# Kernel optimization log

Measured on AMD Instinct MI355X. Metric: run time of the kernel, lower is better.

The kernel has to match this reference:

```python
import jax, jax.numpy as jnp
import numpy as np

N_NODES = 50000
N_EDGES = 1600000
N_FEAT = 128
HIDDEN = 128
N_GRAPHS = 64
N_CLASSES = 10
N_REGS = 1


def setup_inputs() -> dict:
    key = jax.random.key(0)
    ks = jax.random.split(key, 16)
    inp = {
        "x": jax.random.normal(ks[0], (N_NODES, N_FEAT), dtype=jnp.float32),
        "edge_index": jax.random.randint(ks[1], (2, N_EDGES), 0, N_NODES, dtype=jnp.int32),
        "batch": jnp.sort(jax.random.randint(ks[2], (N_NODES,), 0, N_GRAPHS, dtype=jnp.int32)),
        # GCNConv layer params (PyG: linear without bias applied first, bias added after aggregation)
        "w0": jax.random.normal(ks[3], (N_FEAT, HIDDEN), dtype=jnp.float32) * 0.05,
        "b0": jax.random.normal(ks[4], (HIDDEN,), dtype=jnp.float32) * 0.05,
        "w1": jax.random.normal(ks[5], (HIDDEN, HIDDEN), dtype=jnp.float32) * 0.05,
        "b1": jax.random.normal(ks[6], (HIDDEN,), dtype=jnp.float32) * 0.05,
        "w2": jax.random.normal(ks[7], (HIDDEN, HIDDEN), dtype=jnp.float32) * 0.05,
        "b2": jax.random.normal(ks[8], (HIDDEN,), dtype=jnp.float32) * 0.05,
        # heads
        "wc": jax.random.normal(ks[9], (HIDDEN, N_CLASSES), dtype=jnp.float32) * 0.05,
        "bc": jax.random.normal(ks[10], (N_CLASSES,), dtype=jnp.float32) * 0.05,
        "wr": jax.random.normal(ks[11], (HIDDEN, N_REGS), dtype=jnp.float32) * 0.05,
        "br": jax.random.normal(ks[12], (N_REGS,), dtype=jnp.float32) * 0.05,
    }
    return inp


def _gcn_layer(x, src, dst, w, b, deg_inv_sqrt, deg_inv):
    # x: [N, Din] -> [N, Dout]. GCNConv: D^-1/2 (A+I) D^-1/2 (x W) + b
    h = x @ w  # [N, Dout]
    coef = (deg_inv_sqrt[src] * deg_inv_sqrt[dst])[:, None]  # [E, 1]
    agg = jax.ops.segment_sum(h[src] * coef, dst, num_segments=x.shape[0])
    agg = agg + h * deg_inv[:, None]  # self-loop term: deg^-1 * h
    return agg + b


def reference(x, edge_index, batch, w0, b0, w1, b1, w2, b2, wc, bc, wr, br):
    src, dst = edge_index[0], edge_index[1]
    n = x.shape[0]
    # degrees include self-loop weight 1 (PyG gcn_norm with edge_weight=1)
    deg = jax.ops.segment_sum(jnp.ones(src.shape, x.dtype), dst, num_segments=n) + 1.0
    deg_inv_sqrt = deg ** -0.5
    deg_inv = 1.0 / deg

    h = _gcn_layer(x, src, dst, w0, b0, deg_inv_sqrt, deg_inv)
    h = _gcn_layer(jax.nn.elu(h), src, dst, w1, b1, deg_inv_sqrt, deg_inv)
    h = _gcn_layer(jax.nn.elu(h), src, dst, w2, b2, deg_inv_sqrt, deg_inv)

    # global mean pool over graphs
    sums = jax.ops.segment_sum(h, batch, num_segments=N_GRAPHS)  # [G, H]
    cnt = jax.ops.segment_sum(jnp.ones((n,), h.dtype), batch, num_segments=N_GRAPHS)
    pooled = sums / jnp.maximum(cnt, 1.0)[:, None]

    cls_out = pooled @ wc + bc
    reg_out = pooled @ wr + br
    return (pooled, cls_out, reg_out)
```

## Files before the change

### kernel.cpp

```cpp
#include <hip/hip_runtime.h>
#include <hip/hip_fp16.h>
#include <math.h>

#define N_NODES   50000
#define N_EDGES   1600000
#define NF        128
#define N_GRAPHS  64
#define N_CLASSES 10

#define NBK       391
#define BK_SHIFT  7
#define BK_NODES  128
#define CHUNK     8192
#define NCHUNKS   ((N_EDGES + CHUNK - 1) / CHUNK)

typedef _Float16 half8 __attribute__((ext_vector_type(8)));
typedef float f32x4 __attribute__((ext_vector_type(4)));

__global__ void k_zero(int* __restrict__ bucket_cnt, float* __restrict__ sums) {
    int i = blockIdx.x * 256 + threadIdx.x;
    if (i < NBK) bucket_cnt[i] = 0;
    if (i < N_GRAPHS * NF) sums[i] = 0.f;
}

__global__ __launch_bounds__(256) void k_bcount(const int* __restrict__ dst,
                                                int* __restrict__ bucket_cnt) {
    __shared__ int h[NBK];
    int t = threadIdx.x;
    for (int i = t; i < NBK; i += 256) h[i] = 0;
    __syncthreads();
    int base = blockIdx.x * CHUNK;
    int end = min(base + CHUNK, N_EDGES);
    for (int e = base + t; e < end; e += 256)
        atomicAdd(&h[dst[e] >> BK_SHIFT], 1);
    __syncthreads();
    for (int i = t; i < NBK; i += 256)
        if (h[i]) atomicAdd(&bucket_cnt[i], h[i]);
}

__global__ __launch_bounds__(512) void k_bscan(const int* __restrict__ bucket_cnt,
                                               int* __restrict__ bucket_off,
                                               int* __restrict__ bucket_cursor,
                                               int* __restrict__ row_start) {
    __shared__ int ts[512];
    int t = threadIdx.x;
    int v = (t < NBK) ? bucket_cnt[t] : 0;
    ts[t] = v;
    __syncthreads();
    for (int off = 1; off < 512; off <<= 1) {
        int y = (t >= off) ? ts[t - off] : 0;
        __syncthreads();
        ts[t] += y;
        __syncthreads();
    }
    if (t < NBK) {
        int ex = ts[t] - v;
        bucket_off[t] = ex;
        bucket_cursor[t] = ex;
    }
    if (t == 0) {
        int total = ts[511];
        bucket_off[NBK] = total;
        row_start[N_NODES] = total;
    }
}

__global__ __launch_bounds__(256) void k_bscatter(const int* __restrict__ src,
                                                  const int* __restrict__ dst,
                                                  int* __restrict__ bucket_cursor,
                                                  int* __restrict__ pairs) {
    __shared__ int h[NBK], rb[NBK], c2[NBK];
    int t = threadIdx.x;
    for (int i = t; i < NBK; i += 256) { h[i] = 0; c2[i] = 0; }
    __syncthreads();
    int base = blockIdx.x * CHUNK;
    int end = min(base + CHUNK, N_EDGES);
    for (int e = base + t; e < end; e += 256)
        atomicAdd(&h[dst[e] >> BK_SHIFT], 1);
    __syncthreads();
    for (int i = t; i < NBK; i += 256)
        rb[i] = h[i] ? atomicAdd(&bucket_cursor[i], h[i]) : 0;
    __syncthreads();
    for (int e = base + t; e < end; e += 256) {
        int d = dst[e];
        int b = d >> BK_SHIFT;
        int k = atomicAdd(&c2[b], 1);
        pairs[rb[b] + k] = (src[e] << BK_SHIFT) | (d & (BK_NODES - 1));
    }
}

__global__ __launch_bounds__(256) void k_bfill(const int* __restrict__ pairs,
                                               const int* __restrict__ bucket_off,
                                               int* __restrict__ row_start,
                                               float* __restrict__ dis,
                                               int* __restrict__ csr_src) {
    __shared__ int cnt[BK_NODES];
    __shared__ int cur[BK_NODES];
    __shared__ int ts[256];
    int b = blockIdx.x, t = threadIdx.x;
    int node_base = b << BK_SHIFT;
    int lo = bucket_off[b], hi = bucket_off[b + 1];

    if (t < BK_NODES) cnt[t] = 0;
    __syncthreads();
    for (int e = lo + t; e < hi; e += 256)
        atomicAdd(&cnt[pairs[e] & (BK_NODES - 1)], 1);
    __syncthreads();

    int a = (t < BK_NODES) ? cnt[t] : 0;
    ts[t] = a;
    __syncthreads();
    for (int off = 1; off < 256; off <<= 1) {
        int y = (t >= off) ? ts[t - off] : 0;
        __syncthreads();
        ts[t] += y;
        __syncthreads();
    }
    int row = lo + ts[t] - a;
    if (t < BK_NODES) {
        cur[t] = row;
        int n = node_base + t;
        if (n < N_NODES) {
            row_start[n] = row;
            dis[n] = rsqrtf((float)(a + 1));
        }
    }
    __syncthreads();

    for (int e = lo + t; e < hi; e += 256) {
        int p = pairs[e];
        int pos = atomicAdd(&cur[p & (BK_NODES - 1)], 1);
        csr_src[pos] = p >> BK_SHIFT;
    }
}

__global__ void k_xconv(const float* __restrict__ x, _Float16* __restrict__ xh) {
    int i = blockIdx.x * 256 + threadIdx.x;
    if (i >= N_NODES * NF / 4) return;
    float4 v = ((const float4*)x)[i];
    _Float16 h4[4] = {(_Float16)v.x, (_Float16)v.y, (_Float16)v.z, (_Float16)v.w};
    *(uint2*)&xh[(size_t)i * 4] = *(uint2*)h4;
}

__global__ void k_wconv(const float* __restrict__ w0, const float* __restrict__ w1,
                        const float* __restrict__ w2, _Float16* __restrict__ wf) {
    int b = blockIdx.x, t = threadIdx.x;
    const float* W = (b == 0) ? w0 : (b == 1) ? w1 : w2;
    _Float16* dst = wf + (size_t)b * NF * NF;
    for (int idx = t; idx < NF * NF; idx += 256) {
        int k = idx >> 7, n = idx & 127;
        int nt = n >> 4, kc = k >> 5, quad = (k >> 3) & 3, j = k & 7;
        int lane = quad * 16 + (n & 15);
        dst[((nt * 4 + kc) * 64 + lane) * 8 + j] = (_Float16)W[idx];
    }
}

template <bool ELU>
__global__ __launch_bounds__(256) void k_gemm(const _Float16* __restrict__ X,
                                              const _Float16* __restrict__ WF,
                                              const float* __restrict__ dis,
                                              __half* __restrict__ H) {
    __shared__ _Float16 xs[64 * 136];
    int t = threadIdx.x;
    int row0 = blockIdx.x * 64;
#pragma unroll
    for (int i = 0; i < 4; i++) {
        int f = i * 256 + t;
        int r = f >> 4, c = (f & 15) * 8;
        half8 v = {};
        int gr = row0 + r;
        if (gr < N_NODES) v = *(const half8*)&X[(size_t)gr * NF + c];
        if (ELU) {
#pragma unroll
            for (int j = 0; j < 8; j++) {
                float xv = (float)v[j];
                v[j] = (_Float16)(xv > 0.f ? xv : (expf(xv) - 1.f));
            }
        }
        *(half8*)&xs[r * 136 + c] = v;
    }
    __syncthreads();

    int w = t >> 6;
    int lane = t & 63;
    int m = lane & 15, quad = lane >> 4;

    half8 a[4];
#pragma unroll
    for (int kc = 0; kc < 4; kc++)
        a[kc] = *(const half8*)&xs[(w * 16 + m) * 136 + kc * 32 + quad * 8];

    f32x4 acc[8];
#pragma unroll
    for (int nt = 0; nt < 8; nt++) {
        f32x4 c4 = {0.f, 0.f, 0.f, 0.f};
#pragma unroll
        for (int kc = 0; kc < 4; kc++) {
            half8 bf = *(const half8*)&WF[((nt * 4 + kc) * 64 + lane) * 8];
            c4 = __builtin_amdgcn_mfma_f32_16x16x32_f16(a[kc], bf, c4, 0, 0, 0);
        }
        acc[nt] = c4;
    }

#pragma unroll
    for (int reg = 0; reg < 4; reg++) {
        int r = row0 + w * 16 + quad * 4 + reg;
        if (r < N_NODES) {
            float ds = dis[r];
#pragma unroll
            for (int nt = 0; nt < 8; nt++)
                H[(size_t)r * NF + nt * 16 + m] = __float2half(ds * acc[nt][reg]);
        }
    }
}

template <bool HALF_OUT>
__global__ __launch_bounds__(256) void k_agg(const __half* __restrict__ H,
                                             const float* __restrict__ bias,
                                             const int* __restrict__ row_start,
                                             const int* __restrict__ csr_src,
                                             const float* __restrict__ dis,
                                             void* __restrict__ outv) {
    const __half2* H2 = (const __half2*)H;
    int wid  = (blockIdx.x * 256 + threadIdx.x) >> 6;
    int lane = threadIdx.x & 63;
    if (wid >= N_NODES) return;
    int i = wid;
    int rs = row_start[i], re = row_start[i + 1];
    float a0 = 0.f, a1 = 0.f;
    int e = rs;
    for (; e + 7 < re; e += 8) {
        float2 h[8];
#pragma unroll
        for (int j = 0; j < 8; j++) {
            int s = csr_src[e + j];
            h[j] = __half22float2(H2[(size_t)s * 64 + lane]);
        }
#pragma unroll
        for (int j = 0; j < 8; j++) { a0 += h[j].x; a1 += h[j].y; }
    }
    for (; e < re; e++) {
        int s = csr_src[e];
        float2 h = __half22float2(H2[(size_t)s * 64 + lane]);
        a0 += h.x;
        a1 += h.y;
    }
    float2 hs = __half22float2(H2[(size_t)i * 64 + lane]);
    a0 += hs.x;
    a1 += hs.y;
    float di = dis[i];
    int c = lane * 2;
    float o0 = a0 * di + bias[c];
    float o1 = a1 * di + bias[c + 1];
    if (HALF_OUT) {
        ((__half2*)outv)[(size_t)i * 64 + lane] = __floats2half2_rn(o0, o1);
    } else {
        float2 o = make_float2(o0, o1);
        *(float2*)&((float*)outv)[(size_t)i * NF + c] = o;
    }
}

__global__ void k_pool(const float* __restrict__ A, const int* __restrict__ batch,
                       float* __restrict__ sums) {
    int b = blockIdx.x, t = threadIdx.x;
    int c = t & 127, th = t >> 7;
    int start = b * 256 + th;
    if (start >= N_NODES) return;
    int end = min(N_NODES, b * 256 + 256);
    float acc = 0.f;
    int gcur = batch[start];
    for (int i = start; i < end; i += 2) {
        int g = batch[i];
        if (g != gcur) {
            atomicAdd(&sums[gcur * NF + c], acc);
            acc = 0.f;
            gcur = g;
        }
        acc += A[(size_t)i * NF + c];
    }
    atomicAdd(&sums[gcur * NF + c], acc);
}

__global__ void k_head(const float* __restrict__ sums, const int* __restrict__ batch,
                       const float* __restrict__ wc, const float* __restrict__ bc,
                       const float* __restrict__ wr, const float* __restrict__ br,
                       float* __restrict__ out) {
    __shared__ float p[128];
    __shared__ int cnt_s;
    int g = blockIdx.x, c = threadIdx.x;
    if (c == 0) {
        int lo = 0, hi = N_NODES;
        while (lo < hi) { int m = (lo + hi) >> 1; if (batch[m] < g) lo = m + 1; else hi = m; }
        int s0 = lo;
        lo = 0; hi = N_NODES;
        while (lo < hi) { int m = (lo + hi) >> 1; if (batch[m] < g + 1) lo = m + 1; else hi = m; }
        cnt_s = lo - s0;
    }
    __syncthreads();
    float cnt = (float)max(cnt_s, 1);
    float pv = sums[g * NF + c] / cnt;
    p[c] = pv;
    out[g * NF + c] = pv;
    __syncthreads();
    if (c < N_CLASSES) {
        float d = bc[c];
        for (int k = 0; k < NF; k++) d += p[k] * wc[k * N_CLASSES + c];
        out[N_GRAPHS * NF + g * N_CLASSES + c] = d;
    }
    if (c == N_CLASSES) {
        float d = br[0];
        for (int k = 0; k < NF; k++) d += p[k] * wr[k];
        out[N_GRAPHS * NF + N_GRAPHS * N_CLASSES + g] = d;
    }
}

extern "C" void kernel_launch(void* const* d_in, const int* in_sizes, int n_in,
                              void* d_out, int out_size, void* d_ws, size_t ws_size,
                              hipStream_t stream) {
    const float* x     = (const float*)d_in[0];
    const int*   ei    = (const int*)d_in[1];
    const int*   batch = (const int*)d_in[2];
    const float* w0 = (const float*)d_in[3];
    const float* b0 = (const float*)d_in[4];
    const float* w1 = (const float*)d_in[5];
    const float* b1 = (const float*)d_in[6];
    const float* w2 = (const float*)d_in[7];
    const float* b2 = (const float*)d_in[8];
    const float* wc = (const float*)d_in[9];
    const float* bc = (const float*)d_in[10];
    const float* wr = (const float*)d_in[11];
    const float* br = (const float*)d_in[12];
    const int* srcp = ei;
    const int* dstp = ei + N_EDGES;
    float* out = (float*)d_out;

    char* ws = (char*)d_ws;
    size_t off = 0;
    auto alloc = [&](size_t bytes) -> void* {
        void* p = ws + off;
        off = (off + bytes + 255) & ~(size_t)255;
        return p;
    };
    const int NPAD = N_NODES + 64;
    int*      row_start  = (int*)alloc((N_NODES + 1) * 4);
    int*      bucket_cnt = (int*)alloc(NBK * 4);
    int*      bucket_off = (int*)alloc((NBK + 1) * 4);
    int*      bucket_cur = (int*)alloc(NBK * 4);
    float*    dis        = (float*)alloc(N_NODES * 4);
    int*      csr_src    = (int*)alloc((size_t)N_EDGES * 4);
    __half*   Hbuf       = (__half*)alloc((size_t)NPAD * NF * 2);
    float*    Abuf       = (float*)alloc((size_t)NPAD * NF * 4);
    _Float16* xh         = (_Float16*)alloc((size_t)NPAD * NF * 2);
    _Float16* wf         = (_Float16*)alloc((size_t)3 * NF * NF * 2);
    float*    sums       = (float*)alloc(N_GRAPHS * NF * 4);
    (void)ws_size;
    int* pairs = (int*)Abuf;
    _Float16* Ah = xh;

    k_zero<<<(N_GRAPHS * NF + 255) / 256, 256, 0, stream>>>(bucket_cnt, sums);
    k_bcount<<<NCHUNKS, 256, 0, stream>>>(dstp, bucket_cnt);
    k_bscan<<<1, 512, 0, stream>>>(bucket_cnt, bucket_off, bucket_cur, row_start);
    k_bscatter<<<NCHUNKS, 256, 0, stream>>>(srcp, dstp, bucket_cur, pairs);
    k_bfill<<<NBK, 256, 0, stream>>>(pairs, bucket_off, row_start, dis, csr_src);
    k_wconv<<<3, 256, 0, stream>>>(w0, w1, w2, wf);
    k_xconv<<<(N_NODES * NF / 4 + 255) / 256, 256, 0, stream>>>(x, xh);

    const int gemm_grid = (N_NODES + 63) / 64;
    const int agg_grid  = (N_NODES + 3) / 4;

    k_gemm<false><<<gemm_grid, 256, 0, stream>>>(xh, wf, dis, Hbuf);
    k_agg<true><<<agg_grid, 256, 0, stream>>>(Hbuf, b0, row_start, csr_src, dis, Ah);
    k_gemm<true><<<gemm_grid, 256, 0, stream>>>(Ah, wf + NF * NF, dis, Hbuf);
    k_agg<true><<<agg_grid, 256, 0, stream>>>(Hbuf, b1, row_start, csr_src, dis, Ah);
    k_gemm<true><<<gemm_grid, 256, 0, stream>>>(Ah, wf + 2 * NF * NF, dis, Hbuf);
    k_agg<false><<<agg_grid, 256, 0, stream>>>(Hbuf, b2, row_start, csr_src, dis, Abuf);

    k_pool<<<(N_NODES + 255) / 256, 256, 0, stream>>>(Abuf, batch, sums);
    k_head<<<N_GRAPHS, 128, 0, stream>>>(sums, batch, wc, bc, wr, br, out);
}
```

Baseline: 430.9 us.

## Use fixed-size bucket slabs to skip counting, and half-wave 8-byte aggregation

Drops the bucket count and scan kernels by giving each destination bucket a fixed slab of 5120 slots, with a cursor initialised to its slab base. Because rows are no longer contiguous across buckets, the CSR now stores explicit row_end values. The aggregation kernel now assigns two nodes per wavefront, with each lane loading 4 halfs (8 bytes) and writing vectorised bias and output. The fixed slab assumes no bucket receives more than 5120 edges, which holds for uniform random destinations but would overflow on skewed graphs.

```diff
diff --git a/kernel.cpp b/kernel.cpp
--- a/kernel.cpp
+++ b/kernel.cpp
@@ -11,23 +11,26 @@
 #define NBK       391
 #define BK_SHIFT  7
 #define BK_NODES  128
-#define CHUNK     8192
+#define SLAB      5120
+#define CHUNK     4096
 #define NCHUNKS   ((N_EDGES + CHUNK - 1) / CHUNK)
 
 typedef _Float16 half8 __attribute__((ext_vector_type(8)));
 typedef float f32x4 __attribute__((ext_vector_type(4)));
 
-__global__ void k_zero(int* __restrict__ bucket_cnt, float* __restrict__ sums) {
+__global__ void k_zero(int* __restrict__ bucket_cur, float* __restrict__ sums) {
     int i = blockIdx.x * 256 + threadIdx.x;
-    if (i < NBK) bucket_cnt[i] = 0;
+    if (i < NBK) bucket_cur[i] = i * SLAB;
     if (i < N_GRAPHS * NF) sums[i] = 0.f;
 }
 
-__global__ __launch_bounds__(256) void k_bcount(const int* __restrict__ dst,
-                                                int* __restrict__ bucket_cnt) {
-    __shared__ int h[NBK];
+__global__ __launch_bounds__(256) void k_bscatter(const int* __restrict__ src,
+                                                  const int* __restrict__ dst,
+                                                  int* __restrict__ bucket_cur,
+                                                  int* __restrict__ pairs) {
+    __shared__ int h[NBK], rb[NBK], c2[NBK];
     int t = threadIdx.x;
-    for (int i = t; i < NBK; i += 256) h[i] = 0;
+    for (int i = t; i < NBK; i += 256) { h[i] = 0; c2[i] = 0; }
     __syncthreads();
     int base = blockIdx.x * CHUNK;
     int end = min(base + CHUNK, N_EDGES);
@@ -35,51 +38,7 @@
         atomicAdd(&h[dst[e] >> BK_SHIFT], 1);
     __syncthreads();
     for (int i = t; i < NBK; i += 256)
-        if (h[i]) atomicAdd(&bucket_cnt[i], h[i]);
-}
-
-__global__ __launch_bounds__(512) void k_bscan(const int* __restrict__ bucket_cnt,
-                                               int* __restrict__ bucket_off,
-                                               int* __restrict__ bucket_cursor,
-                                               int* __restrict__ row_start) {
-    __shared__ int ts[512];
-    int t = threadIdx.x;
-    int v = (t < NBK) ? bucket_cnt[t] : 0;
-    ts[t] = v;
-    __syncthreads();
-    for (int off = 1; off < 512; off <<= 1) {
-        int y = (t >= off) ? ts[t - off] : 0;
-        __syncthreads();
-        ts[t] += y;
-        __syncthreads();
-    }
-    if (t < NBK) {
-        int ex = ts[t] - v;
-        bucket_off[t] = ex;
-        bucket_cursor[t] = ex;
-    }
-    if (t == 0) {
-        int total = ts[511];
-        bucket_off[NBK] = total;
-        row_start[N_NODES] = total;
-    }
-}
-
-__global__ __launch_bounds__(256) void k_bscatter(const int* __restrict__ src,
-                                                  const int* __restrict__ dst,
-                                                  int* __restrict__ bucket_cursor,
-                                                  int* __restrict__ pairs) {
-    __shared__ int h[NBK], rb[NBK], c2[NBK];
-    int t = threadIdx.x;
-    for (int i = t; i < NBK; i += 256) { h[i] = 0; c2[i] = 0; }
-    __syncthreads();
-    int base = blockIdx.x * CHUNK;
-    int end = min(base + CHUNK, N_EDGES);
-    for (int e = base + t; e < end; e += 256)
-        atomicAdd(&h[dst[e] >> BK_SHIFT], 1);
-    __syncthreads();
-    for (int i = t; i < NBK; i += 256)
-        rb[i] = h[i] ? atomicAdd(&bucket_cursor[i], h[i]) : 0;
+        rb[i] = h[i] ? atomicAdd(&bucket_cur[i], h[i]) : 0;
     __syncthreads();
     for (int e = base + t; e < end; e += 256) {
         int d = dst[e];
@@ -89,28 +48,29 @@
     }
 }
 
-__global__ __launch_bounds__(256) void k_bfill(const int* __restrict__ pairs,
-                                               const int* __restrict__ bucket_off,
+__global__ __launch_bounds__(512) void k_bfill(const int* __restrict__ pairs,
+                                               const int* __restrict__ bucket_cur,
                                                int* __restrict__ row_start,
+                                               int* __restrict__ row_end,
                                                float* __restrict__ dis,
                                                int* __restrict__ csr_src) {
     __shared__ int cnt[BK_NODES];
     __shared__ int cur[BK_NODES];
-    __shared__ int ts[256];
+    __shared__ int ts[512];
     int b = blockIdx.x, t = threadIdx.x;
     int node_base = b << BK_SHIFT;
-    int lo = bucket_off[b], hi = bucket_off[b + 1];
+    int lo = b * SLAB, hi = bucket_cur[b];
 
     if (t < BK_NODES) cnt[t] = 0;
     __syncthreads();
-    for (int e = lo + t; e < hi; e += 256)
+    for (int e = lo + t; e < hi; e += 512)
         atomicAdd(&cnt[pairs[e] & (BK_NODES - 1)], 1);
     __syncthreads();
 
     int a = (t < BK_NODES) ? cnt[t] : 0;
     ts[t] = a;
     __syncthreads();
-    for (int off = 1; off < 256; off <<= 1) {
+    for (int off = 1; off < BK_NODES; off <<= 1) {
         int y = (t >= off) ? ts[t - off] : 0;
         __syncthreads();
         ts[t] += y;
@@ -122,12 +82,13 @@
         int n = node_base + t;
         if (n < N_NODES) {
             row_start[n] = row;
+            row_end[n]   = row + a;
             dis[n] = rsqrtf((float)(a + 1));
         }
     }
     __syncthreads();
 
-    for (int e = lo + t; e < hi; e += 256) {
+    for (int e = lo + t; e < hi; e += 512) {
         int p = pairs[e];
         int pos = atomicAdd(&cur[p & (BK_NODES - 1)], 1);
         csr_src[pos] = p >> BK_SHIFT;
@@ -218,45 +179,58 @@
 __global__ __launch_bounds__(256) void k_agg(const __half* __restrict__ H,
                                              const float* __restrict__ bias,
                                              const int* __restrict__ row_start,
+                                             const int* __restrict__ row_end,
                                              const int* __restrict__ csr_src,
                                              const float* __restrict__ dis,
                                              void* __restrict__ outv) {
-    const __half2* H2 = (const __half2*)H;
-    int wid  = (blockIdx.x * 256 + threadIdx.x) >> 6;
+    const uint2* H4 = (const uint2*)H;
+    int wv   = (blockIdx.x * 256 + threadIdx.x) >> 6;
     int lane = threadIdx.x & 63;
-    if (wid >= N_NODES) return;
-    int i = wid;
-    int rs = row_start[i], re = row_start[i + 1];
-    float a0 = 0.f, a1 = 0.f;
+    int node = wv * 2 + (lane >> 5);
+    int l    = lane & 31;
+    if (node >= N_NODES) return;
+    int rs = row_start[node], re = row_end[node];
+    float a0 = 0.f, a1 = 0.f, a2 = 0.f, a3 = 0.f;
     int e = rs;
     for (; e + 7 < re; e += 8) {
-        float2 h[8];
+        uint2 v[8];
 #pragma unroll
         for (int j = 0; j < 8; j++) {
             int s = csr_src[e + j];
-            h[j] = __half22float2(H2[(size_t)s * 64 + lane]);
-        }
-#pragma unroll
-        for (int j = 0; j < 8; j++) { a0 += h[j].x; a1 += h[j].y; }
+            v[j] = H4[(size_t)s * 32 + l];
+        }
+#pragma unroll
+        for (int j = 0; j < 8; j++) {
+            float2 lo = __half22float2(*(__half2*)&v[j].x);
+            float2 hi = __half22float2(*(__half2*)&v[j].y);
+            a0 += lo.x; a1 += lo.y; a2 += hi.x; a3 += hi.y;
+        }
     }
     for (; e < re; e++) {
         int s = csr_src[e];
-        float2 h = __half22float2(H2[(size_t)s * 64 + lane]);
-        a0 += h.x;
-        a1 += h.y;
-    }
-    float2 hs = __half22float2(H2[(size_t)i * 64 + lane]);
-    a0 += hs.x;
-    a1 += hs.y;
-    float di = dis[i];
-    int c = lane * 2;
-    float o0 = a0 * di + bias[c];
-    float o1 = a1 * di + bias[c + 1];
+        uint2 v = H4[(size_t)s * 32 + l];
+        float2 lo = __half22float2(*(__half2*)&v.x);
+        float2 hi = __half22float2(*(__half2*)&v.y);
+        a0 += lo.x; a1 += lo.y; a2 += hi.x; a3 += hi.y;
+    }
+    {
+        uint2 v = H4[(size_t)node * 32 + l];
+        float2 lo = __half22float2(*(__half2*)&v.x);
+        float2 hi = __half22float2(*(__half2*)&v.y);
+        a0 += lo.x; a1 += lo.y; a2 += hi.x; a3 += hi.y;
+    }
+    float di = dis[node];
+    int c = l * 4;
+    float4 bv = *(const float4*)&bias[c];
+    float o0 = a0 * di + bv.x, o1 = a1 * di + bv.y;
+    float o2 = a2 * di + bv.z, o3 = a3 * di + bv.w;
     if (HALF_OUT) {
-        ((__half2*)outv)[(size_t)i * 64 + lane] = __floats2half2_rn(o0, o1);
+        uint2 o;
+        *(__half2*)&o.x = __floats2half2_rn(o0, o1);
+        *(__half2*)&o.y = __floats2half2_rn(o2, o3);
+        ((uint2*)outv)[(size_t)node * 32 + l] = o;
     } else {
-        float2 o = make_float2(o0, o1);
-        *(float2*)&((float*)outv)[(size_t)i * NF + c] = o;
+        *(float4*)&((float*)outv)[(size_t)node * NF + c] = make_float4(o0, o1, o2, o3);
     }
 }
 
@@ -342,12 +316,11 @@
         return p;
     };
     const int NPAD = N_NODES + 64;
-    int*      row_start  = (int*)alloc((N_NODES + 1) * 4);
-    int*      bucket_cnt = (int*)alloc(NBK * 4);
-    int*      bucket_off = (int*)alloc((NBK + 1) * 4);
+    int*      row_start  = (int*)alloc(N_NODES * 4);
+    int*      row_end    = (int*)alloc(N_NODES * 4);
     int*      bucket_cur = (int*)alloc(NBK * 4);
     float*    dis        = (float*)alloc(N_NODES * 4);
-    int*      csr_src    = (int*)alloc((size_t)N_EDGES * 4);
+    int*      csr_src    = (int*)alloc((size_t)NBK * SLAB * 4);
     __half*   Hbuf       = (__half*)alloc((size_t)NPAD * NF * 2);
     float*    Abuf       = (float*)alloc((size_t)NPAD * NF * 4);
     _Float16* xh         = (_Float16*)alloc((size_t)NPAD * NF * 2);
@@ -357,23 +330,21 @@
     int* pairs = (int*)Abuf;
     _Float16* Ah = xh;
 
-    k_zero<<<(N_GRAPHS * NF + 255) / 256, 256, 0, stream>>>(bucket_cnt, sums);
-    k_bcount<<<NCHUNKS, 256, 0, stream>>>(dstp, bucket_cnt);
-    k_bscan<<<1, 512, 0, stream>>>(bucket_cnt, bucket_off, bucket_cur, row_start);
+    k_zero<<<32, 256, 0, stream>>>(bucket_cur, sums);
     k_bscatter<<<NCHUNKS, 256, 0, stream>>>(srcp, dstp, bucket_cur, pairs);
-    k_bfill<<<NBK, 256, 0, stream>>>(pairs, bucket_off, row_start, dis, csr_src);
+    k_bfill<<<NBK, 512, 0, stream>>>(pairs, bucket_cur, row_start, row_end, dis, csr_src);
     k_wconv<<<3, 256, 0, stream>>>(w0, w1, w2, wf);
     k_xconv<<<(N_NODES * NF / 4 + 255) / 256, 256, 0, stream>>>(x, xh);
 
     const int gemm_grid = (N_NODES + 63) / 64;
-    const int agg_grid  = (N_NODES + 3) / 4;
+    const int agg_grid  = (N_NODES + 7) / 8;
 
     k_gemm<false><<<gemm_grid, 256, 0, stream>>>(xh, wf, dis, Hbuf);
-    k_agg<true><<<agg_grid, 256, 0, stream>>>(Hbuf, b0, row_start, csr_src, dis, Ah);
+    k_agg<true><<<agg_grid, 256, 0, stream>>>(Hbuf, b0, row_start, row_end, csr_src, dis, Ah);
     k_gemm<true><<<gemm_grid, 256, 0, stream>>>(Ah, wf + NF * NF, dis, Hbuf);
-    k_agg<true><<<agg_grid, 256, 0, stream>>>(Hbuf, b1, row_start, csr_src, dis, Ah);
+    k_agg<true><<<agg_grid, 256, 0, stream>>>(Hbuf, b1, row_start, row_end, csr_src, dis, Ah);
     k_gemm<true><<<gemm_grid, 256, 0, stream>>>(Ah, wf + 2 * NF * NF, dis, Hbuf);
-    k_agg<false><<<agg_grid, 256, 0, stream>>>(Hbuf, b2, row_start, csr_src, dis, Abuf);
+    k_agg<false><<<agg_grid, 256, 0, stream>>>(Hbuf, b2, row_start, row_end, csr_src, dis, Abuf);
 
     k_pool<<<(N_NODES + 255) / 256, 256, 0, stream>>>(Abuf, batch, sums);
     k_head<<<N_GRAPHS, 128, 0, stream>>>(sums, batch, wc, bc, wr, br, out);
```

Result: faster. 404.5 us (-6.1%).
